# Kernel tuning notes

Hardware: AMD Instinct MI355X
Metric: run time of the kernel (lower is better)

The kernel has to match this reference:

```python
import jax, jax.numpy as jnp
import numpy as np

B, T, I, H, K = 128, 1024, 64, 128, 3


def setup_inputs() -> dict:
    key = jax.random.key(0)
    ks = jax.random.split(key, 20)
    stdv = 1.0 / np.sqrt(H)
    u = lambda k, shape: jax.random.uniform(k, shape, jnp.float32, -stdv, stdv)
    return {
        "Y": jax.random.normal(ks[0], (B, T, I), jnp.float32),
        "aux": jax.random.normal(ks[1], (K, B, T, I), jnp.float32),
        "W_i": u(ks[2], (I, H)), "U_i": u(ks[3], (H, H)), "b_i": u(ks[4], (H,)),
        "W_f": u(ks[5], (I, H)), "U_f": u(ks[6], (H, H)), "b_f": u(ks[7], (H,)),
        "W_c": u(ks[8], (I, H)), "U_c": u(ks[9], (H, H)), "b_c": u(ks[10], (H,)),
        "W_o": u(ks[11], (I, H)), "U_o": u(ks[12], (H, H)), "b_o": u(ks[13], (H,)),
        "aux_W": u(ks[14], (K, I, H)), "aux_b": u(ks[15], (K, H)),
        "W_a": u(ks[16], (H, H)), "b_a": u(ks[17], (H,)),
    }


def reference(Y, aux, W_i, U_i, b_i, W_f, U_f, b_f, W_c, U_c, b_c,
              W_o, U_o, b_o, aux_W, aux_b, W_a, b_a):
    # Precompute all input-to-hidden projections (no h dependence) -> time-major [T,B,H]
    xi = jnp.einsum('bti,ih->tbh', Y, W_i) + b_i
    xf = jnp.einsum('bti,ih->tbh', Y, W_f) + b_f
    xc = jnp.einsum('bti,ih->tbh', Y, W_c) + b_c
    xo = jnp.einsum('bti,ih->tbh', Y, W_o) + b_o
    # Aux gate outputs: tanh(Linear(aux_t)) per factor -> [T,K,B,H]
    aux_p = jnp.tanh(jnp.einsum('kbti,kih->tkbh', aux, aux_W) + aux_b[:, None, :])

    bs = Y.shape[0]
    h0 = jnp.zeros((bs, W_i.shape[1]), Y.dtype)
    c0 = jnp.zeros_like(h0)

    def step(carry, xs):
        h, c = carry
        xi_t, xf_t, xc_t, xo_t, aux_t = xs
        i_t = jax.nn.sigmoid(xi_t + h @ U_i)
        f_t = jax.nn.sigmoid(xf_t + h @ U_f)
        C_tilde = jnp.tanh(xc_t + h @ U_c)
        o_t = jax.nn.sigmoid(xo_t + h @ U_o)
        combined = jnp.concatenate([C_tilde[None], aux_t], axis=0)  # [K+1,B,H]
        w = jax.nn.softmax(combined @ W_a + b_a, axis=0)
        L_t = jnp.sum(w * combined, axis=0)
        c_new = f_t * c + i_t * L_t
        h_new = o_t * jnp.tanh(c_new)
        return (h_new, c_new), h_new

    (h_t, _), hs = jax.lax.scan(step, (h0, c0), (xi, xf, xc, xo, aux_p))
    return h_t, jnp.transpose(hs, (1, 0, 2))  # (h_t [B,H], hidden_seq [B,T,H])
```

## Files before the change

### kernel.cpp

```cpp
#include <hip/hip_runtime.h>
#include <hip/hip_bf16.h>

#define Bb 128
#define Tt 1024
#define Ii 64
#define Hh 128

typedef float v2f __attribute__((ext_vector_type(2)));
static __device__ __forceinline__ v2f mk2(float x, float y) { v2f r; r.x = x; r.y = y; return r; }
static __device__ __forceinline__ float sigmoidf_(float x) { return 1.f / (1.f + expf(-x)); }


__launch_bounds__(256, 1)
__global__ void p1_gates(const float* __restrict__ Y,
                         const float* __restrict__ Wi, const float* __restrict__ Wf,
                         const float* __restrict__ Wc, const float* __restrict__ Wo,
                         const float* __restrict__ bi, const float* __restrict__ bff,
                         const float* __restrict__ bc, const float* __restrict__ bo,
                         float* __restrict__ Xc, int t0) {
  const int b   = blockIdx.x & 127;
  const int tt  = blockIdx.x >> 7;
  const int tg  = t0 + tt * 32;
  const int tlb = tt * 32;
  const int tau = threadIdx.x;

  __shared__ float wlds[64][512];
  __shared__ float yin[32][64];
  __shared__ float blds[512];

  {
    const float* Ws[4] = {Wi, Wf, Wc, Wo};
#pragma unroll
    for (int g = 0; g < 4; ++g) {
      const float4* src = (const float4*)Ws[g];
#pragma unroll
      for (int it = 0; it < 8; ++it) {
        int idx = it * 256 + tau;
        int k = idx >> 5, c4 = idx & 31;
        *(float4*)&wlds[k][g * 128 + c4 * 4] = src[idx];
      }
    }
    if (tau < 128) {
      blds[0 * 128 + tau] = bi[tau];
      blds[1 * 128 + tau] = bff[tau];
      blds[2 * 128 + tau] = bc[tau];
      blds[3 * 128 + tau] = bo[tau];
    }
    const float4* ys = (const float4*)(Y + ((size_t)b * Tt + tg) * Ii);
    ((float4*)&yin[0][0])[tau]       = ys[tau];
    ((float4*)&yin[0][0])[tau + 256] = ys[tau + 256];
  }
  __syncthreads();

  const int cp = tau;
  v2f acc[32];
#pragma unroll
  for (int r = 0; r < 32; ++r) acc[r] = mk2(0.f, 0.f);

#pragma unroll
  for (int k4 = 0; k4 < 16; ++k4) {
    v2f w0 = *(const v2f*)&wlds[k4 * 4 + 0][2 * cp];
    v2f w1 = *(const v2f*)&wlds[k4 * 4 + 1][2 * cp];
    v2f w2 = *(const v2f*)&wlds[k4 * 4 + 2][2 * cp];
    v2f w3 = *(const v2f*)&wlds[k4 * 4 + 3][2 * cp];
#pragma unroll
    for (int r = 0; r < 32; ++r) {
      float4 y = *(const float4*)&yin[r][k4 * 4];
      acc[r] += w0 * y.x;  acc[r] += w1 * y.y;
      acc[r] += w2 * y.z;  acc[r] += w3 * y.w;
    }
  }

  v2f bb = *(const v2f*)&blds[2 * cp];
#pragma unroll
  for (int r = 0; r < 32; ++r) {
    size_t base = ((size_t)(tlb + r) * Bb + b) * 768;
    *(v2f*)&Xc[base + 2 * cp] = acc[r] + bb;
  }
}

__launch_bounds__(256, 1)
__global__ void p2_aux(const float* __restrict__ aux,
                       const float* __restrict__ auxW, const float* __restrict__ auxb,
                       const float* __restrict__ Wa, const float* __restrict__ ba,
                       float* __restrict__ Xc, int t0) {
  const int b   = blockIdx.x & 127;
  const int tt  = blockIdx.x >> 7;
  const int tg  = t0 + tt * 16;
  const int tlb = tt * 16;
  const int tau = threadIdx.x;

  __shared__ float awlds[3][64][128];
  __shared__ float ain[3][16][64];
  __shared__ float am[3][16][128];
  __shared__ float bstage[512];

  {
    const float4* src = (const float4*)auxW;
#pragma unroll
    for (int it = 0; it < 24; ++it) {
      int idx = it * 256 + tau;
      ((float4*)&awlds[0][0][0])[idx] = src[idx];
    }
#pragma unroll
    for (int m = 0; m < 3; ++m) {
      const float4* as = (const float4*)(aux + (((size_t)m * Bb + b) * Tt + tg) * Ii);
      ((float4*)&ain[m][0][0])[tau] = as[tau];
    }
    if (tau < 128) {
      bstage[0 * 128 + tau] = auxb[0 * 128 + tau];
      bstage[1 * 128 + tau] = auxb[1 * 128 + tau];
      bstage[2 * 128 + tau] = auxb[2 * 128 + tau];
      bstage[384 + tau]     = ba[tau];
    }
  }
  __syncthreads();

  {
    const int j  = tau & 127;
    const int rh = tau >> 7;
#pragma unroll
    for (int m = 0; m < 3; ++m) {
      float a8[8];
#pragma unroll
      for (int r = 0; r < 8; ++r) a8[r] = 0.f;
#pragma unroll
      for (int k4 = 0; k4 < 16; ++k4) {
        float w0 = awlds[m][k4 * 4 + 0][j];
        float w1 = awlds[m][k4 * 4 + 1][j];
        float w2 = awlds[m][k4 * 4 + 2][j];
        float w3 = awlds[m][k4 * 4 + 3][j];
#pragma unroll
        for (int r = 0; r < 8; ++r) {
          float4 x = *(const float4*)&ain[m][rh * 8 + r][k4 * 4];
          a8[r] += x.x * w0 + x.y * w1 + x.z * w2 + x.w * w3;
        }
      }
      float bmj = bstage[m * 128 + j];
#pragma unroll
      for (int r = 0; r < 8; ++r) am[m][rh * 8 + r][j] = tanhf(a8[r] + bmj);
    }
  }
  __syncthreads();

  {
    const int jj = tau >> 1;
    const int s2 = tau & 1;
    v2f wa2[32];
#pragma unroll
    for (int p = 0; p < 32; ++p) {
      int k = s2 * 64 + 2 * p;
      wa2[p] = mk2(Wa[(size_t)k * Hh + jj], Wa[(size_t)(k + 1) * Hh + jj]);
    }
    const float baj = bstage[384 + jj];
#pragma unroll
    for (int r = 0; r < 16; ++r) {
      v2f a0 = mk2(0.f, 0.f), a1 = mk2(0.f, 0.f), a2 = mk2(0.f, 0.f);
#pragma unroll
      for (int k2 = 0; k2 < 32; ++k2) {
        v2f x0 = *(const v2f*)&am[0][r][s2 * 64 + 2 * k2];
        v2f x1 = *(const v2f*)&am[1][r][s2 * 64 + 2 * k2];
        v2f x2 = *(const v2f*)&am[2][r][s2 * 64 + 2 * k2];
        a0 += wa2[k2] * x0;  a1 += wa2[k2] * x1;  a2 += wa2[k2] * x2;
      }
      float v0 = a0.x + a0.y, v1 = a1.x + a1.y, v2 = a2.x + a2.y;
      v0 += __shfl_xor(v0, 1);
      v1 += __shfl_xor(v1, 1);
      v2 += __shfl_xor(v2, 1);
      if (s2 == 0) {
        float e0 = expf(v0 + baj);
        float e1 = expf(v1 + baj);
        float e2 = expf(v2 + baj);
        float S3 = e0 + e1 + e2;
        float N3 = e0 * am[0][r][jj] + e1 * am[1][r][jj] + e2 * am[2][r][jj];
        size_t base = ((size_t)(tlb + r) * Bb + b) * 768;
        Xc[base + 512 + jj] = S3;
        Xc[base + 640 + jj] = N3;
      }
    }
  }
}

__launch_bounds__(1024, 4)
__global__ void scan3(const float* __restrict__ Xc,
                      const float* __restrict__ Ui, const float* __restrict__ Uf,
                      const float* __restrict__ Uc, const float* __restrict__ Uo,
                      const float* __restrict__ Wa, const float* __restrict__ ba,
                      float* __restrict__ state, float* __restrict__ out,
                      int t0, int Cc) {
  const int b   = blockIdx.x;
  const int tau = threadIdx.x;

  const int gA = tau >> 8;
  const int jA = (tau >> 1) & 127;
  const int sA = tau & 1;
  const int jC = tau >> 3;
  const int rC = tau & 7;
  const int jD = tau & 127;

  __shared__ float hbuf[Hh];
  __shared__ float act[4][Hh];
  __shared__ float v0buf[Hh];

  const float* Ug = (gA == 0) ? Ui : (gA == 1) ? Uf : (gA == 2) ? Uc : Uo;
  v2f wu[32];
#pragma unroll
  for (int p = 0; p < 32; ++p) {
    int k = sA * 64 + 2 * p;
    wu[p] = mk2(Ug[(size_t)k * Hh + jA], Ug[(size_t)(k + 1) * Hh + jA]);
  }
  v2f wa2[8];
#pragma unroll
  for (int p = 0; p < 8; ++p) {
    int k = rC * 16 + 2 * p;
    wa2[p] = mk2(Wa[(size_t)k * Hh + jC], Wa[(size_t)(k + 1) * Hh + jC]);
  }
  const float ba_j = ba[jD];

  float c = 0.f, h = 0.f;
  if (tau < Hh) {
    if (t0 > 0) { h = state[b * 256 + tau]; c = state[b * 256 + 128 + tau]; }
    hbuf[tau] = h;
  }

  float xg_cur = Xc[((size_t)0 * Bb + b) * 768 + gA * Hh + jA];
  float s3_cur = 0.f, n3_cur = 0.f;
  if (tau < Hh) {
    s3_cur = Xc[((size_t)0 * Bb + b) * 768 + 512 + jD];
    n3_cur = Xc[((size_t)0 * Bb + b) * 768 + 640 + jD];
  }
  __syncthreads();

  for (int tl = 0; tl < Cc; ++tl) {
    float xg_nx = 0.f, s3_nx = 0.f, n3_nx = 0.f;
    if (tl + 1 < Cc) {
      size_t nb = ((size_t)(tl + 1) * Bb + b) * 768;
      xg_nx = Xc[nb + gA * Hh + jA];
      if (tau < Hh) { s3_nx = Xc[nb + 512 + jD]; n3_nx = Xc[nb + 640 + jD]; }
    }

    v2f acc = mk2(0.f, 0.f);
#pragma unroll
    for (int q4 = 0; q4 < 16; ++q4) {
      float4 h4 = *(const float4*)&hbuf[sA * 64 + q4 * 4];
      acc += wu[2 * q4]     * mk2(h4.x, h4.y);
      acc += wu[2 * q4 + 1] * mk2(h4.z, h4.w);
    }
    float dot = acc.x + acc.y;
    dot += __shfl_xor(dot, 1);
    if (sA == 0) {
      float pre = dot + xg_cur;
      act[gA][jA] = (gA == 2) ? tanhf(pre) : sigmoidf_(pre);
    }
    __syncthreads();

    v2f vacc = mk2(0.f, 0.f);
#pragma unroll
    for (int p4 = 0; p4 < 4; ++p4) {
      float4 c4 = *(const float4*)&act[2][rC * 16 + p4 * 4];
      vacc += wa2[2 * p4]     * mk2(c4.x, c4.y);
      vacc += wa2[2 * p4 + 1] * mk2(c4.z, c4.w);
    }
    float v = vacc.x + vacc.y;
    v += __shfl_xor(v, 1);
    v += __shfl_xor(v, 2);
    v += __shfl_xor(v, 4);
    if (rC == 0) v0buf[jC] = v;
    __syncthreads();

    if (tau < Hh) {
      float e0 = expf(v0buf[jD] + ba_j);
      float ct = act[2][jD];
      float L  = (e0 * ct + n3_cur) / (e0 + s3_cur);
      c = act[1][jD] * c + act[0][jD] * L;
      h = act[3][jD] * tanhf(c);
      hbuf[jD] = h;
      out[16384 + ((size_t)b * Tt + (t0 + tl)) * Hh + jD] = h;
      if (t0 + tl == Tt - 1) out[(size_t)b * Hh + jD] = h;
    }
    __syncthreads();

    xg_cur = xg_nx;  s3_cur = s3_nx;  n3_cur = n3_nx;
  }

  if (tau < Hh) {
    state[b * 256 + tau] = h;
    state[b * 256 + 128 + tau] = c;
  }
}

__launch_bounds__(512, 2)
__global__ void fused_kernel(const float* __restrict__ Y,
                             const float* __restrict__ aux,
                             const float* __restrict__ Wi, const float* __restrict__ Ui,
                             const float* __restrict__ bi,
                             const float* __restrict__ Wf, const float* __restrict__ Uf,
                             const float* __restrict__ bfp,
                             const float* __restrict__ Wc, const float* __restrict__ Uc,
                             const float* __restrict__ bc,
                             const float* __restrict__ Wo, const float* __restrict__ Uo,
                             const float* __restrict__ bo,
                             const float* __restrict__ auxW, const float* __restrict__ auxb,
                             const float* __restrict__ Wa, const float* __restrict__ ba,
                             float* __restrict__ out) {
  const int b   = blockIdx.x;
  const int tau = threadIdx.x;
  const int j   = tau & 127;
  const int q   = tau >> 7;

  __shared__ float wG[4][Ii][Hh];
  __shared__ float xraw[2][4][Ii];
  __shared__ float hbuf[Hh];
  __shared__ float ctl[Hh];
  __shared__ float auxp[3][Hh];
  __shared__ float redG[4][4][Hh];
  __shared__ float redX[3][4][Hh];

  float wU[4][32];
  {
    const float* Us[4] = {Ui, Uf, Uc, Uo};
#pragma unroll
    for (int g = 0; g < 4; ++g)
#pragma unroll
      for (int k = 0; k < 32; ++k)
        wU[g][k] = Us[g][(q * 32 + k) * Hh + j];
  }
  float wA[32];
#pragma unroll
  for (int k = 0; k < 32; ++k) wA[k] = Wa[(q * 32 + k) * Hh + j];
  float wAux[3][16];
#pragma unroll
  for (int m = 0; m < 3; ++m)
#pragma unroll
    for (int k = 0; k < 16; ++k)
      wAux[m][k] = auxW[((size_t)m * Ii + (q * 16 + k)) * Hh + j];
  float bgate[4];
  {
    const float* Bs[4] = {bi, bfp, bc, bo};
#pragma unroll
    for (int g = 0; g < 4; ++g) bgate[g] = Bs[g][j];
  }
  const float abias = (q >= 1) ? auxb[(q - 1) * Hh + j] : 0.f;
  const float ba_j  = ba[j];

  {
    const float* Ws[4] = {Wi, Wf, Wc, Wo};
#pragma unroll
    for (int g = 0; g < 4; ++g) {
      const float4* src = (const float4*)Ws[g];
      float4* dst = (float4*)&wG[g][0][0];
#pragma unroll
      for (int r = 0; r < 4; ++r) dst[tau + r * 512] = src[tau + r * 512];
    }
  }

  if (tau < Hh) hbuf[tau] = 0.f;
  float c = 0.f;

  const bool ldr = (tau < 64);
  const int  m4  = tau >> 4;
  const int  idx = tau & 15;
  const float* srcbase = nullptr;
  float4 xn = make_float4(0.f, 0.f, 0.f, 0.f);
  if (ldr) {
    srcbase = (m4 == 0) ? (Y + ((size_t)b * Tt) * Ii)
                        : (aux + (((size_t)(m4 - 1) * Bb + b) * Tt) * Ii);
    float4 x0 = ((const float4*)srcbase)[idx];
    ((float4*)&xraw[0][0][0])[tau] = x0;
    xn = ((const float4*)(srcbase + Ii))[idx];
  }
  __syncthreads();

  for (int t = 0; t < Tt; ++t) {
    const int p = t & 1;
    float aG0 = 0.f, aG1 = 0.f, aG2 = 0.f, aG3 = 0.f;
#pragma unroll
    for (int kk = 0; kk < 8; ++kk) {
      float4 hv = *(const float4*)&hbuf[q * 32 + kk * 4];
      aG0 += hv.x*wU[0][kk*4] + hv.y*wU[0][kk*4+1] + hv.z*wU[0][kk*4+2] + hv.w*wU[0][kk*4+3];
      aG1 += hv.x*wU[1][kk*4] + hv.y*wU[1][kk*4+1] + hv.z*wU[1][kk*4+2] + hv.w*wU[1][kk*4+3];
      aG2 += hv.x*wU[2][kk*4] + hv.y*wU[2][kk*4+1] + hv.z*wU[2][kk*4+2] + hv.w*wU[2][kk*4+3];
      aG3 += hv.x*wU[3][kk*4] + hv.y*wU[3][kk*4+1] + hv.z*wU[3][kk*4+2] + hv.w*wU[3][kk*4+3];
    }
#pragma unroll
    for (int kk = 0; kk < 4; ++kk) {
      const int k0 = q * 16 + kk * 4;
      float4 yv = *(const float4*)&xraw[p][0][k0];
      aG0 += yv.x*wG[0][k0][j] + yv.y*wG[0][k0+1][j] + yv.z*wG[0][k0+2][j] + yv.w*wG[0][k0+3][j];
      aG1 += yv.x*wG[1][k0][j] + yv.y*wG[1][k0+1][j] + yv.z*wG[1][k0+2][j] + yv.w*wG[1][k0+3][j];
      aG2 += yv.x*wG[2][k0][j] + yv.y*wG[2][k0+1][j] + yv.z*wG[2][k0+2][j] + yv.w*wG[2][k0+3][j];
      aG3 += yv.x*wG[3][k0][j] + yv.y*wG[3][k0+1][j] + yv.z*wG[3][k0+2][j] + yv.w*wG[3][k0+3][j];
    }
    float sA0 = 0.f, sA1 = 0.f, sA2 = 0.f;
#pragma unroll
    for (int kk = 0; kk < 4; ++kk) {
      const int k0 = q * 16 + kk * 4;
      float4 a0v = *(const float4*)&xraw[p][1][k0];
      float4 a1v = *(const float4*)&xraw[p][2][k0];
      float4 a2v = *(const float4*)&xraw[p][3][k0];
      sA0 += a0v.x*wAux[0][kk*4] + a0v.y*wAux[0][kk*4+1] + a0v.z*wAux[0][kk*4+2] + a0v.w*wAux[0][kk*4+3];
      sA1 += a1v.x*wAux[1][kk*4] + a1v.y*wAux[1][kk*4+1] + a1v.z*wAux[1][kk*4+2] + a1v.w*wAux[1][kk*4+3];
      sA2 += a2v.x*wAux[2][kk*4] + a2v.y*wAux[2][kk*4+1] + a2v.z*wAux[2][kk*4+2] + a2v.w*wAux[2][kk*4+3];
    }
    redG[0][q][j] = aG0;  redG[1][q][j] = aG1;
    redG[2][q][j] = aG2;  redG[3][q][j] = aG3;
    redX[0][q][j] = sA0;  redX[1][q][j] = sA1;  redX[2][q][j] = sA2;
    __syncthreads();

    if (q == 0) {
      float pi = bgate[0] + redG[0][0][j] + redG[0][1][j] + redG[0][2][j] + redG[0][3][j];
      float pf = bgate[1] + redG[1][0][j] + redG[1][1][j] + redG[1][2][j] + redG[1][3][j];
      float pc = bgate[2] + redG[2][0][j] + redG[2][1][j] + redG[2][2][j] + redG[2][3][j];
      float po = bgate[3] + redG[3][0][j] + redG[3][1][j] + redG[3][2][j] + redG[3][3][j];
      float ig = sigmoidf_(pi);
      float fg = sigmoidf_(pf);
      float og = sigmoidf_(po);
      ctl[j] = tanhf(pc);
      redG[0][0][j] = ig;  redG[1][0][j] = fg;  redG[3][0][j] = og;
    } else {
      const int m = q - 1;
      float v = abias + redX[m][0][j] + redX[m][1][j] + redX[m][2][j] + redX[m][3][j];
      auxp[m][j] = tanhf(v);
    }
    if (ldr) {
      ((float4*)&xraw[p ^ 1][0][0])[tau] = xn;
      if (t + 2 < Tt) xn = ((const float4*)(srcbase + (size_t)(t + 2) * Ii))[idx];
    }
    __syncthreads();

    float sS0 = 0.f, sS1 = 0.f, sS2 = 0.f, sS3 = 0.f;
#pragma unroll
    for (int kk = 0; kk < 8; ++kk) {
      const int k0 = q * 32 + kk * 4;
      float4 c0 = *(const float4*)&ctl[k0];
      float4 c1 = *(const float4*)&auxp[0][k0];
      float4 c2 = *(const float4*)&auxp[1][k0];
      float4 c3 = *(const float4*)&auxp[2][k0];
      sS0 += c0.x*wA[kk*4] + c0.y*wA[kk*4+1] + c0.z*wA[kk*4+2] + c0.w*wA[kk*4+3];
      sS1 += c1.x*wA[kk*4] + c1.y*wA[kk*4+1] + c1.z*wA[kk*4+2] + c1.w*wA[kk*4+3];
      sS2 += c2.x*wA[kk*4] + c2.y*wA[kk*4+1] + c2.z*wA[kk*4+2] + c2.w*wA[kk*4+3];
      sS3 += c3.x*wA[kk*4] + c3.y*wA[kk*4+1] + c3.z*wA[kk*4+2] + c3.w*wA[kk*4+3];
    }
    __syncthreads();
    redX[0][q][j] = sS1;  redX[1][q][j] = sS2;  redX[2][q][j] = sS3;
    redG[2][q][j] = sS0;
    __syncthreads();

    if (q == 0) {
      float v0 = ba_j + redG[2][0][j] + redG[2][1][j] + redG[2][2][j] + redG[2][3][j];
      float v1 = ba_j + redX[0][0][j] + redX[0][1][j] + redX[0][2][j] + redX[0][3][j];
      float v2 = ba_j + redX[1][0][j] + redX[1][1][j] + redX[1][2][j] + redX[1][3][j];
      float v3 = ba_j + redX[2][0][j] + redX[2][1][j] + redX[2][2][j] + redX[2][3][j];
      float mx = fmaxf(fmaxf(v0, v1), fmaxf(v2, v3));
      float e0 = expf(v0 - mx), e1 = expf(v1 - mx), e2 = expf(v2 - mx), e3 = expf(v3 - mx);
      float inv = 1.f / (e0 + e1 + e2 + e3);
      float L = (e0 * ctl[j] + e1 * auxp[0][j] + e2 * auxp[1][j] + e3 * auxp[2][j]) * inv;
      float ig = redG[0][0][j], fg = redG[1][0][j], og = redG[3][0][j];
      c = fg * c + ig * L;
      float h = og * tanhf(c);
      hbuf[j] = h;
      out[16384 + ((size_t)b * Tt + t) * Hh + j] = h;
      if (t == Tt - 1) out[(size_t)b * Hh + j] = h;
    }
    __syncthreads();
  }
}

extern "C" void kernel_launch(void* const* d_in, const int* in_sizes, int n_in,
                              void* d_out, int out_size, void* d_ws, size_t ws_size,
                              hipStream_t stream) {
  (void)in_sizes; (void)n_in; (void)out_size;
  const float* Y     = (const float*)d_in[0];
  const float* aux   = (const float*)d_in[1];
  const float* W_i   = (const float*)d_in[2];
  const float* U_i   = (const float*)d_in[3];
  const float* b_i   = (const float*)d_in[4];
  const float* W_f   = (const float*)d_in[5];
  const float* U_f   = (const float*)d_in[6];
  const float* b_f   = (const float*)d_in[7];
  const float* W_c   = (const float*)d_in[8];
  const float* U_c   = (const float*)d_in[9];
  const float* b_c   = (const float*)d_in[10];
  const float* W_o   = (const float*)d_in[11];
  const float* U_o   = (const float*)d_in[12];
  const float* b_o   = (const float*)d_in[13];
  const float* aux_W = (const float*)d_in[14];
  const float* aux_b = (const float*)d_in[15];
  const float* W_a   = (const float*)d_in[16];
  const float* b_a   = (const float*)d_in[17];
  float* out = (float*)d_out;

  int C = 0;
  const int cands[4] = {512, 256, 128, 64};
  for (int i = 0; i < 4; ++i) {
    size_t need = (size_t)cands[i] * Bb * 768 * sizeof(float) + 131072;
    if (d_ws != nullptr && ws_size >= need) { C = cands[i]; break; }
  }

  if (C > 0) {
    float* Xc    = (float*)d_ws;
    float* state = (float*)((char*)d_ws + (size_t)C * Bb * 768 * sizeof(float));
    for (int t0 = 0; t0 < Tt; t0 += C) {
      int Cc = (Tt - t0 < C) ? (Tt - t0) : C;
      p1_gates<<<dim3(Bb * (Cc / 32)), dim3(256), 0, stream>>>(
          Y, W_i, W_f, W_c, W_o, b_i, b_f, b_c, b_o, Xc, t0);
      p2_aux<<<dim3(Bb * (Cc / 16)), dim3(256), 0, stream>>>(
          aux, aux_W, aux_b, W_a, b_a, Xc, t0);
      scan3<<<dim3(Bb), dim3(1024), 0, stream>>>(
          Xc, U_i, U_f, U_c, U_o, W_a, b_a, state, out, t0, Cc);
    }
  } else {
    fused_kernel<<<dim3(Bb), dim3(512), 0, stream>>>(
        Y, aux, W_i, U_i, b_i, W_f, U_f, b_f, W_c, U_c, b_c,
        W_o, U_o, b_o, aux_W, aux_b, W_a, b_a, out);
  }
}
```

Measured before the change: 3.353 ms.

## Make projection kernels persistent and restructure scan to 512 threads per batch

The gate and aux projection kernels become persistent grids of 256 blocks that loop over tiles, so the weights are staged into shared memory once per block rather than once per tile. The scan kernel drops from 1024 to 512 threads: each thread computes a full 128-length dot product for one gate column, which removes one shuffle reduction and one barrier per timestep, and the softmax-weight reduction is split four ways. The time-chunk candidate list gains 1024, allowing a single pass when the workspace is large enough. The trade-off is more serial work per thread in the latency-bound scan and 128 registers held per thread for the U weights.

```diff
diff --git a/kernel.cpp b/kernel.cpp
--- a/kernel.cpp
+++ b/kernel.cpp
@@ -17,16 +17,12 @@
                          const float* __restrict__ Wc, const float* __restrict__ Wo,
                          const float* __restrict__ bi, const float* __restrict__ bff,
                          const float* __restrict__ bc, const float* __restrict__ bo,
-                         float* __restrict__ Xc, int t0) {
-  const int b   = blockIdx.x & 127;
-  const int tt  = blockIdx.x >> 7;
-  const int tg  = t0 + tt * 32;
-  const int tlb = tt * 32;
+                         float* __restrict__ Xc, int t0, int ntiles) {
   const int tau = threadIdx.x;
 
   __shared__ float wlds[64][512];
+  __shared__ float blds[512];
   __shared__ float yin[32][64];
-  __shared__ float blds[512];
 
   {
     const float* Ws[4] = {Wi, Wf, Wc, Wo};
@@ -46,36 +42,44 @@
       blds[2 * 128 + tau] = bc[tau];
       blds[3 * 128 + tau] = bo[tau];
     }
+  }
+
+  for (int tile = blockIdx.x; tile < ntiles; tile += 256) {
+    const int b   = tile & 127;
+    const int tt  = tile >> 7;
+    const int tg  = t0 + tt * 32;
+    const int tlb = tt * 32;
+
     const float4* ys = (const float4*)(Y + ((size_t)b * Tt + tg) * Ii);
     ((float4*)&yin[0][0])[tau]       = ys[tau];
     ((float4*)&yin[0][0])[tau + 256] = ys[tau + 256];
-  }
-  __syncthreads();
-
-  const int cp = tau;
-  v2f acc[32];
-#pragma unroll
-  for (int r = 0; r < 32; ++r) acc[r] = mk2(0.f, 0.f);
-
-#pragma unroll
-  for (int k4 = 0; k4 < 16; ++k4) {
-    v2f w0 = *(const v2f*)&wlds[k4 * 4 + 0][2 * cp];
-    v2f w1 = *(const v2f*)&wlds[k4 * 4 + 1][2 * cp];
-    v2f w2 = *(const v2f*)&wlds[k4 * 4 + 2][2 * cp];
-    v2f w3 = *(const v2f*)&wlds[k4 * 4 + 3][2 * cp];
+    __syncthreads();
+
+    v2f acc[32];
+#pragma unroll
+    for (int r = 0; r < 32; ++r) acc[r] = mk2(0.f, 0.f);
+
+#pragma unroll
+    for (int k4 = 0; k4 < 16; ++k4) {
+      v2f w0 = *(const v2f*)&wlds[k4 * 4 + 0][2 * tau];
+      v2f w1 = *(const v2f*)&wlds[k4 * 4 + 1][2 * tau];
+      v2f w2 = *(const v2f*)&wlds[k4 * 4 + 2][2 * tau];
+      v2f w3 = *(const v2f*)&wlds[k4 * 4 + 3][2 * tau];
+#pragma unroll
+      for (int r = 0; r < 32; ++r) {
+        float4 y = *(const float4*)&yin[r][k4 * 4];
+        acc[r] += w0 * y.x;  acc[r] += w1 * y.y;
+        acc[r] += w2 * y.z;  acc[r] += w3 * y.w;
+      }
+    }
+
+    v2f bb = *(const v2f*)&blds[2 * tau];
 #pragma unroll
     for (int r = 0; r < 32; ++r) {
-      float4 y = *(const float4*)&yin[r][k4 * 4];
-      acc[r] += w0 * y.x;  acc[r] += w1 * y.y;
-      acc[r] += w2 * y.z;  acc[r] += w3 * y.w;
-    }
-  }
-
-  v2f bb = *(const v2f*)&blds[2 * cp];
-#pragma unroll
-  for (int r = 0; r < 32; ++r) {
-    size_t base = ((size_t)(tlb + r) * Bb + b) * 768;
-    *(v2f*)&Xc[base + 2 * cp] = acc[r] + bb;
+      size_t base = ((size_t)(tlb + r) * Bb + b) * 768;
+      *(v2f*)&Xc[base + 2 * tau] = acc[r] + bb;
+    }
+    __syncthreads();
   }
 }
 
@@ -83,17 +87,13 @@
 __global__ void p2_aux(const float* __restrict__ aux,
                        const float* __restrict__ auxW, const float* __restrict__ auxb,
                        const float* __restrict__ Wa, const float* __restrict__ ba,
-                       float* __restrict__ Xc, int t0) {
-  const int b   = blockIdx.x & 127;
-  const int tt  = blockIdx.x >> 7;
-  const int tg  = t0 + tt * 16;
-  const int tlb = tt * 16;
+                       float* __restrict__ Xc, int t0, int ntiles) {
   const int tau = threadIdx.x;
 
   __shared__ float awlds[3][64][128];
+  __shared__ float am[3][16][128];
   __shared__ float ain[3][16][64];
-  __shared__ float am[3][16][128];
-  __shared__ float bstage[512];
+  __shared__ float bst[384];
 
   {
     const float4* src = (const float4*)auxW;
@@ -102,23 +102,39 @@
       int idx = it * 256 + tau;
       ((float4*)&awlds[0][0][0])[idx] = src[idx];
     }
+    if (tau < 128) {
+      bst[0 * 128 + tau] = auxb[0 * 128 + tau];
+      bst[1 * 128 + tau] = auxb[1 * 128 + tau];
+      bst[2 * 128 + tau] = auxb[2 * 128 + tau];
+    }
+  }
+
+  const int jj = tau >> 1;
+  const int s2 = tau & 1;
+  v2f wa2[32];
+#pragma unroll
+  for (int p = 0; p < 32; ++p) {
+    int k = s2 * 64 + 2 * p;
+    wa2[p] = mk2(Wa[(size_t)k * Hh + jj], Wa[(size_t)(k + 1) * Hh + jj]);
+  }
+  const float baj = ba[jj];
+
+  const int j  = tau & 127;
+  const int rh = tau >> 7;
+
+  for (int tile = blockIdx.x; tile < ntiles; tile += 256) {
+    const int b   = tile & 127;
+    const int tt  = tile >> 7;
+    const int tg  = t0 + tt * 16;
+    const int tlb = tt * 16;
+
 #pragma unroll
     for (int m = 0; m < 3; ++m) {
       const float4* as = (const float4*)(aux + (((size_t)m * Bb + b) * Tt + tg) * Ii);
       ((float4*)&ain[m][0][0])[tau] = as[tau];
     }
-    if (tau < 128) {
-      bstage[0 * 128 + tau] = auxb[0 * 128 + tau];
-      bstage[1 * 128 + tau] = auxb[1 * 128 + tau];
-      bstage[2 * 128 + tau] = auxb[2 * 128 + tau];
-      bstage[384 + tau]     = ba[tau];
-    }
-  }
-  __syncthreads();
-
-  {
-    const int j  = tau & 127;
-    const int rh = tau >> 7;
+    __syncthreads();
+
 #pragma unroll
     for (int m = 0; m < 3; ++m) {
       float a8[8];
@@ -136,32 +152,23 @@
           a8[r] += x.x * w0 + x.y * w1 + x.z * w2 + x.w * w3;
         }
       }
-      float bmj = bstage[m * 128 + j];
+      float bmj = bst[m * 128 + j];
 #pragma unroll
       for (int r = 0; r < 8; ++r) am[m][rh * 8 + r][j] = tanhf(a8[r] + bmj);
     }
-  }
-  __syncthreads();
-
-  {
-    const int jj = tau >> 1;
-    const int s2 = tau & 1;
-    v2f wa2[32];
-#pragma unroll
-    for (int p = 0; p < 32; ++p) {
-      int k = s2 * 64 + 2 * p;
-      wa2[p] = mk2(Wa[(size_t)k * Hh + jj], Wa[(size_t)(k + 1) * Hh + jj]);
-    }
-    const float baj = bstage[384 + jj];
+    __syncthreads();
+
 #pragma unroll
     for (int r = 0; r < 16; ++r) {
       v2f a0 = mk2(0.f, 0.f), a1 = mk2(0.f, 0.f), a2 = mk2(0.f, 0.f);
 #pragma unroll
-      for (int k2 = 0; k2 < 32; ++k2) {
-        v2f x0 = *(const v2f*)&am[0][r][s2 * 64 + 2 * k2];
-        v2f x1 = *(const v2f*)&am[1][r][s2 * 64 + 2 * k2];
-        v2f x2 = *(const v2f*)&am[2][r][s2 * 64 + 2 * k2];
-        a0 += wa2[k2] * x0;  a1 += wa2[k2] * x1;  a2 += wa2[k2] * x2;
+      for (int k4 = 0; k4 < 16; ++k4) {
+        float4 x0 = *(const float4*)&am[0][r][s2 * 64 + k4 * 4];
+        float4 x1 = *(const float4*)&am[1][r][s2 * 64 + k4 * 4];
+        float4 x2 = *(const float4*)&am[2][r][s2 * 64 + k4 * 4];
+        a0 += wa2[2*k4] * mk2(x0.x, x0.y);  a0 += wa2[2*k4+1] * mk2(x0.z, x0.w);
+        a1 += wa2[2*k4] * mk2(x1.x, x1.y);  a1 += wa2[2*k4+1] * mk2(x1.z, x1.w);
+        a2 += wa2[2*k4] * mk2(x2.x, x2.y);  a2 += wa2[2*k4+1] * mk2(x2.z, x2.w);
       }
       float v0 = a0.x + a0.y, v1 = a1.x + a1.y, v2 = a2.x + a2.y;
       v0 += __shfl_xor(v0, 1);
@@ -171,18 +178,17 @@
         float e0 = expf(v0 + baj);
         float e1 = expf(v1 + baj);
         float e2 = expf(v2 + baj);
-        float S3 = e0 + e1 + e2;
-        float N3 = e0 * am[0][r][jj] + e1 * am[1][r][jj] + e2 * am[2][r][jj];
         size_t base = ((size_t)(tlb + r) * Bb + b) * 768;
-        Xc[base + 512 + jj] = S3;
-        Xc[base + 640 + jj] = N3;
+        Xc[base + 512 + jj] = e0 + e1 + e2;
+        Xc[base + 640 + jj] = e0 * am[0][r][jj] + e1 * am[1][r][jj] + e2 * am[2][r][jj];
       }
     }
+    __syncthreads();
   }
 }
 
-__launch_bounds__(1024, 4)
-__global__ void scan3(const float* __restrict__ Xc,
+__launch_bounds__(512, 1)
+__global__ void scan4(const float* __restrict__ Xc,
                       const float* __restrict__ Ui, const float* __restrict__ Uf,
                       const float* __restrict__ Uc, const float* __restrict__ Uo,
                       const float* __restrict__ Wa, const float* __restrict__ ba,
@@ -190,44 +196,37 @@
                       int t0, int Cc) {
   const int b   = blockIdx.x;
   const int tau = threadIdx.x;
-
-  const int gA = tau >> 8;
-  const int jA = (tau >> 1) & 127;
-  const int sA = tau & 1;
-  const int jC = tau >> 3;
-  const int rC = tau & 7;
-  const int jD = tau & 127;
+  const int g   = tau >> 7;
+  const int j   = tau & 127;
+  const int jq  = tau >> 2;
+  const int q   = tau & 3;
 
   __shared__ float hbuf[Hh];
   __shared__ float act[4][Hh];
-  __shared__ float v0buf[Hh];
-
-  const float* Ug = (gA == 0) ? Ui : (gA == 1) ? Uf : (gA == 2) ? Uc : Uo;
-  v2f wu[32];
-#pragma unroll
-  for (int p = 0; p < 32; ++p) {
-    int k = sA * 64 + 2 * p;
-    wu[p] = mk2(Ug[(size_t)k * Hh + jA], Ug[(size_t)(k + 1) * Hh + jA]);
-  }
-  v2f wa2[8];
-#pragma unroll
-  for (int p = 0; p < 8; ++p) {
-    int k = rC * 16 + 2 * p;
-    wa2[p] = mk2(Wa[(size_t)k * Hh + jC], Wa[(size_t)(k + 1) * Hh + jC]);
-  }
-  const float ba_j = ba[jD];
+
+  const float* Ug = (g == 0) ? Ui : (g == 1) ? Uf : (g == 2) ? Uc : Uo;
+  v2f wu[64];
+#pragma unroll
+  for (int p = 0; p < 64; ++p)
+    wu[p] = mk2(Ug[(size_t)(2 * p) * Hh + j], Ug[(size_t)(2 * p + 1) * Hh + j]);
+
+  v2f wa4[16];
+#pragma unroll
+  for (int p = 0; p < 16; ++p) {
+    int k = q * 32 + 2 * p;
+    wa4[p] = mk2(Wa[(size_t)k * Hh + jq], Wa[(size_t)(k + 1) * Hh + jq]);
+  }
+  const float ba_q = ba[jq];
 
   float c = 0.f, h = 0.f;
-  if (tau < Hh) {
-    if (t0 > 0) { h = state[b * 256 + tau]; c = state[b * 256 + 128 + tau]; }
-    hbuf[tau] = h;
-  }
-
-  float xg_cur = Xc[((size_t)0 * Bb + b) * 768 + gA * Hh + jA];
+  if (t0 > 0 && q == 0) c = state[b * 256 + 128 + jq];
+  if (tau < Hh) hbuf[tau] = (t0 > 0) ? state[b * 256 + tau] : 0.f;
+
+  float xg_cur = Xc[(size_t)b * 768 + tau];
   float s3_cur = 0.f, n3_cur = 0.f;
-  if (tau < Hh) {
-    s3_cur = Xc[((size_t)0 * Bb + b) * 768 + 512 + jD];
-    n3_cur = Xc[((size_t)0 * Bb + b) * 768 + 640 + jD];
+  if (q == 0) {
+    s3_cur = Xc[(size_t)b * 768 + 512 + jq];
+    n3_cur = Xc[(size_t)b * 768 + 640 + jq];
   }
   __syncthreads();
 
@@ -235,57 +234,49 @@
     float xg_nx = 0.f, s3_nx = 0.f, n3_nx = 0.f;
     if (tl + 1 < Cc) {
       size_t nb = ((size_t)(tl + 1) * Bb + b) * 768;
-      xg_nx = Xc[nb + gA * Hh + jA];
-      if (tau < Hh) { s3_nx = Xc[nb + 512 + jD]; n3_nx = Xc[nb + 640 + jD]; }
+      xg_nx = Xc[nb + tau];
+      if (q == 0) { s3_nx = Xc[nb + 512 + jq]; n3_nx = Xc[nb + 640 + jq]; }
     }
 
     v2f acc = mk2(0.f, 0.f);
 #pragma unroll
-    for (int q4 = 0; q4 < 16; ++q4) {
-      float4 h4 = *(const float4*)&hbuf[sA * 64 + q4 * 4];
-      acc += wu[2 * q4]     * mk2(h4.x, h4.y);
-      acc += wu[2 * q4 + 1] * mk2(h4.z, h4.w);
-    }
-    float dot = acc.x + acc.y;
-    dot += __shfl_xor(dot, 1);
-    if (sA == 0) {
-      float pre = dot + xg_cur;
-      act[gA][jA] = (gA == 2) ? tanhf(pre) : sigmoidf_(pre);
-    }
-    __syncthreads();
-
-    v2f vacc = mk2(0.f, 0.f);
-#pragma unroll
-    for (int p4 = 0; p4 < 4; ++p4) {
-      float4 c4 = *(const float4*)&act[2][rC * 16 + p4 * 4];
-      vacc += wa2[2 * p4]     * mk2(c4.x, c4.y);
-      vacc += wa2[2 * p4 + 1] * mk2(c4.z, c4.w);
-    }
-    float v = vacc.x + vacc.y;
+    for (int p4 = 0; p4 < 32; ++p4) {
+      float4 h4 = *(const float4*)&hbuf[p4 * 4];
+      acc += wu[2 * p4]     * mk2(h4.x, h4.y);
+      acc += wu[2 * p4 + 1] * mk2(h4.z, h4.w);
+    }
+    float pre = acc.x + acc.y + xg_cur;
+    act[g][j] = (g == 2) ? tanhf(pre) : sigmoidf_(pre);
+    __syncthreads();
+
+    v2f vac = mk2(0.f, 0.f);
+#pragma unroll
+    for (int k4 = 0; k4 < 8; ++k4) {
+      float4 c4 = *(const float4*)&act[2][q * 32 + k4 * 4];
+      vac += wa4[2 * k4]     * mk2(c4.x, c4.y);
+      vac += wa4[2 * k4 + 1] * mk2(c4.z, c4.w);
+    }
+    float v = vac.x + vac.y;
     v += __shfl_xor(v, 1);
     v += __shfl_xor(v, 2);
-    v += __shfl_xor(v, 4);
-    if (rC == 0) v0buf[jC] = v;
-    __syncthreads();
-
-    if (tau < Hh) {
-      float e0 = expf(v0buf[jD] + ba_j);
-      float ct = act[2][jD];
+    if (q == 0) {
+      float e0 = expf(v + ba_q);
+      float ct = act[2][jq];
       float L  = (e0 * ct + n3_cur) / (e0 + s3_cur);
-      c = act[1][jD] * c + act[0][jD] * L;
-      h = act[3][jD] * tanhf(c);
-      hbuf[jD] = h;
-      out[16384 + ((size_t)b * Tt + (t0 + tl)) * Hh + jD] = h;
-      if (t0 + tl == Tt - 1) out[(size_t)b * Hh + jD] = h;
+      c = act[1][jq] * c + act[0][jq] * L;
+      h = act[3][jq] * tanhf(c);
+      hbuf[jq] = h;
+      out[16384 + ((size_t)b * Tt + (t0 + tl)) * Hh + jq] = h;
+      if (t0 + tl == Tt - 1) out[(size_t)b * Hh + jq] = h;
     }
     __syncthreads();
 
     xg_cur = xg_nx;  s3_cur = s3_nx;  n3_cur = n3_nx;
   }
 
-  if (tau < Hh) {
-    state[b * 256 + tau] = h;
-    state[b * 256 + 128 + tau] = c;
+  if (q == 0) {
+    state[b * 256 + jq] = h;
+    state[b * 256 + 128 + jq] = c;
   }
 }
 
@@ -491,8 +482,8 @@
   float* out = (float*)d_out;
 
   int C = 0;
-  const int cands[4] = {512, 256, 128, 64};
-  for (int i = 0; i < 4; ++i) {
+  const int cands[5] = {1024, 512, 256, 128, 64};
+  for (int i = 0; i < 5; ++i) {
     size_t need = (size_t)cands[i] * Bb * 768 * sizeof(float) + 131072;
     if (d_ws != nullptr && ws_size >= need) { C = cands[i]; break; }
   }
@@ -502,11 +493,11 @@
     float* state = (float*)((char*)d_ws + (size_t)C * Bb * 768 * sizeof(float));
     for (int t0 = 0; t0 < Tt; t0 += C) {
       int Cc = (Tt - t0 < C) ? (Tt - t0) : C;
-      p1_gates<<<dim3(Bb * (Cc / 32)), dim3(256), 0, stream>>>(
-          Y, W_i, W_f, W_c, W_o, b_i, b_f, b_c, b_o, Xc, t0);
-      p2_aux<<<dim3(Bb * (Cc / 16)), dim3(256), 0, stream>>>(
-          aux, aux_W, aux_b, W_a, b_a, Xc, t0);
-      scan3<<<dim3(Bb), dim3(1024), 0, stream>>>(
+      p1_gates<<<dim3(256), dim3(256), 0, stream>>>(
+          Y, W_i, W_f, W_c, W_o, b_i, b_f, b_c, b_o, Xc, t0, Bb * (Cc / 32));
+      p2_aux<<<dim3(256), dim3(256), 0, stream>>>(
+          aux, aux_W, aux_b, W_a, b_a, Xc, t0, Bb * (Cc / 16));
+      scan4<<<dim3(Bb), dim3(512), 0, stream>>>(
           Xc, U_i, U_f, U_c, U_o, W_a, b_a, state, out, t0, Cc);
     }
   } else {
```

New measurement: 4.028 ms. 1.2x slower.
